# Kernel optimization log

Measured on AMD Instinct MI355X. Metric: run time of the kernel, lower is better.

## Reference

```python
import jax, jax.numpy as jnp
import numpy as np
from jax import lax

B, L, D_IN, D_H = 4096, 64, 256, 200


def setup_inputs() -> dict:
    key = jax.random.key(0)
    ks = jax.random.split(key, 9)
    s_in = 1.0 / np.sqrt(D_IN)
    s_cv = 1.0 / np.sqrt(D_IN * 4)
    return {
        "x": jax.random.normal(ks[0], (B, L, D_IN), dtype=jnp.float32),
        "Wq": jax.random.uniform(ks[1], (D_H, D_IN), jnp.float32, -s_in, s_in),
        "bq": jax.random.uniform(ks[2], (D_H,), jnp.float32, -s_in, s_in),
        "Wk": jax.random.uniform(ks[3], (D_H, D_IN), jnp.float32, -s_in, s_in),
        "bk": jax.random.uniform(ks[4], (D_H,), jnp.float32, -s_in, s_in),
        "Wv": jax.random.uniform(ks[5], (D_H, D_IN), jnp.float32, -s_in, s_in),
        "bv": jax.random.uniform(ks[6], (D_H,), jnp.float32, -s_in, s_in),
        "conv_w": jax.random.uniform(ks[7], (D_H, D_IN, 4), jnp.float32, -s_cv, s_cv),
        "conv_b": jax.random.uniform(ks[8], (D_H,), jnp.float32, -s_cv, s_cv),
    }


def reference(x, Wq, bq, Wk, bk, Wv, bv, conv_w, conv_b):
    # x: [B, L=64, 256]
    q = jax.nn.relu(jnp.einsum("bld,hd->blh", x, Wq) + bq)  # [B,L,200]
    k = jax.nn.relu(jnp.einsum("bld,hd->blh", x, Wk) + bk)  # relu commutes with permute
    v = jax.nn.relu(jnp.einsum("bld,hd->blh", x, Wv) + bv)
    scores = jnp.einsum("blh,bmh->blm", q, k)               # bmm(q, k^T): [B,L,L]
    soft = jax.nn.softmax(scores, axis=1)                   # NOTE: dim=1 (over queries), as in original
    self_att = jnp.einsum("blm,bmh->blh", soft, v)          # [B,L,200]
    b = x.shape[0]
    self_att = self_att.reshape(b, -1, 4, 16).mean(axis=2).reshape(b, 16, -1)  # [B,16,200]
    word_att = x.reshape(b, 256, 64)                        # [B, C=256, len=64]
    conv = lax.conv_general_dilated(
        word_att, conv_w, window_strides=(4,), padding="VALID",
        dimension_numbers=("NCH", "OIH", "NCH"))            # [B,200,16]
    conv = conv + conv_b[None, :, None]
    conv = conv.reshape(b, 16, -1)                          # raw reshape, as in original
    return conv + self_att                                  # [B,16,200]
```

## Files before the change

kernel.cpp:

```cpp
#include <hip/hip_runtime.h>

typedef _Float16 f16x8 __attribute__((ext_vector_type(8)));
typedef _Float16 f16x4 __attribute__((ext_vector_type(4)));
typedef float f32x4 __attribute__((ext_vector_type(4)));

#define THREADS 512

static __device__ __forceinline__ f32x4 MFMA(f16x8 a, f16x8 b, f32x4 c) {
  return __builtin_amdgcn_mfma_f32_16x16x32_f16(a, b, c, 0, 0, 0);
}

__global__ void wcvt(const float* __restrict__ Wq, const float* __restrict__ Wk,
                     const float* __restrict__ Wv, const float* __restrict__ cw,
                     const float* __restrict__ bq, const float* __restrict__ bk,
                     const float* __restrict__ bv,
                     _Float16* __restrict__ Wb,
                     _Float16* __restrict__ Wcb,
                     float* __restrict__ biasp) {
  int gt = blockIdx.x * blockDim.x + threadIdx.x;
  int gs = gridDim.x * blockDim.x;
  const int WN = 224 * 256;
  for (int i = gt; i < WN; i += gs) {
    int n = i >> 8;
    Wb[i]          = (n < 200) ? (_Float16)Wq[i] : (_Float16)0.f;
    Wb[WN + i]     = (n < 200) ? (_Float16)Wk[i] : (_Float16)0.f;
    Wb[2 * WN + i] = (n < 200) ? (_Float16)Wv[i] : (_Float16)0.f;
  }
  for (int i = gt; i < 224 * 1024; i += gs) {
    int o = i >> 10;
    Wcb[i] = (o < 200) ? (_Float16)cw[i] : (_Float16)0.f;
  }
  for (int i = gt; i < 224; i += gs) {
    biasp[i]       = (i < 200) ? bq[i] : 0.f;
    biasp[224 + i] = (i < 200) ? bk[i] : 0.f;
    biasp[448 + i] = (i < 200) ? bv[i] : 0.f;
  }
}

#define LDS_BYTES 151296

__global__ __launch_bounds__(THREADS, 2) void fused_kernel(
    const float* __restrict__ x, const _Float16* __restrict__ Wb,
    const _Float16* __restrict__ Wcb, const float* __restrict__ biasp,
    const float* __restrict__ convb, float* __restrict__ out) {
  extern __shared__ char smem[];
  _Float16* Xl = (_Float16*)smem;
  _Float16* Qs = (_Float16*)(smem + 33792);
  _Float16* Ks = (_Float16*)(smem + 63488);
  _Float16* Vt = (_Float16*)(smem + 93184);
  float* Sf    = (float*)(smem + 125440);
  _Float16* Sb = (_Float16*)(smem + 142080);
  float* SA    = (float*)(smem + 33792);
  float* Cv    = (float*)(smem + 125440);

  const int b = blockIdx.x;
  const int tid = threadIdx.x;
  const int lane = tid & 63;
  const int wave = tid >> 6;
  const int li = lane & 15;
  const int g = lane >> 4;

  const float* xb = x + (size_t)b * 16384;
  for (int i = tid; i < 4096; i += THREADS) {
    float4 v = ((const float4*)xb)[i];
    int e = i * 4;
    int l = e >> 8, d = e & 255;
    f16x4 h;
    h.x = (_Float16)v.x; h.y = (_Float16)v.y;
    h.z = (_Float16)v.z; h.w = (_Float16)v.w;
    *(f16x4*)(Xl + l * 264 + d) = h;
  }
  __syncthreads();

  for (int u = wave; u < 42; u += 8) {
    int p = u / 14, nt = u % 14;
    int n = nt * 16 + li;
    const _Float16* wrow = Wb + p * (224 * 256) + n * 256 + 8 * g;
    f16x8 bfr[8];
#pragma unroll
    for (int kk = 0; kk < 8; kk++) bfr[kk] = *(const f16x8*)(wrow + kk * 32);
    float bias = biasp[p * 224 + n];
    for (int m = 0; m < 4; m++) {
      f32x4 acc = {0.f, 0.f, 0.f, 0.f};
      const _Float16* arow = Xl + (m * 16 + li) * 264 + 8 * g;
#pragma unroll
      for (int kk = 0; kk < 8; kk++) {
        acc = MFMA(*(const f16x8*)(arow + kk * 32), bfr[kk], acc);
      }
#pragma unroll
      for (int r = 0; r < 4; r++) {
        int row = m * 16 + 4 * g + r;
        float v = acc[r] + bias;
        v = v > 0.f ? v : 0.f;
        _Float16 hv = (_Float16)v;
        if (p == 0) Qs[row * 232 + n] = hv;
        else if (p == 1) Ks[row * 232 + n] = hv;
        else Vt[n * 72 + row] = hv;
      }
    }
  }
  __syncthreads();

  for (int t = wave * 2; t < wave * 2 + 2; t++) {
    int mt = t >> 2, nt = t & 3;
    f32x4 acc = {0.f, 0.f, 0.f, 0.f};
    const _Float16* qrow = Qs + (mt * 16 + li) * 232 + 8 * g;
    const _Float16* krow = Ks + (nt * 16 + li) * 232 + 8 * g;
#pragma unroll
    for (int kk = 0; kk < 7; kk++) {
      acc = MFMA(*(const f16x8*)(qrow + kk * 32),
                 *(const f16x8*)(krow + kk * 32), acc);
    }
#pragma unroll
    for (int r = 0; r < 4; r++) {
      int row = mt * 16 + 4 * g + r;
      int col = nt * 16 + li;
      Sf[row * 65 + col] = acc[r];
    }
  }
  __syncthreads();

  {
    int m = tid >> 3, r = tid & 7;
    float vals[8];
    float mx = -1e30f;
#pragma unroll
    for (int i = 0; i < 8; i++) {
      float v = Sf[(r + 8 * i) * 65 + m];
      vals[i] = v;
      mx = fmaxf(mx, v);
    }
    mx = fmaxf(mx, __shfl_xor(mx, 1));
    mx = fmaxf(mx, __shfl_xor(mx, 2));
    mx = fmaxf(mx, __shfl_xor(mx, 4));
    float s = 0.f;
#pragma unroll
    for (int i = 0; i < 8; i++) {
      vals[i] = __expf(vals[i] - mx);
      s += vals[i];
    }
    s += __shfl_xor(s, 1);
    s += __shfl_xor(s, 2);
    s += __shfl_xor(s, 4);
    float inv = 1.0f / s;
#pragma unroll
    for (int i = 0; i < 8; i++)
      Sb[(r + 8 * i) * 72 + m] = (_Float16)(vals[i] * inv);
  }
  __syncthreads();

  for (int nt = wave; nt < 14; nt += 8) {
    int o = nt * 16 + li;
    const _Float16* wrow = Wcb + o * 1024 + 8 * g;
    f32x4 acc = {0.f, 0.f, 0.f, 0.f};
#pragma unroll 4
    for (int kk = 0; kk < 32; kk++) {
      int i1 = kk * 8 + 2 * g;
      int i2 = i1 + 1;
      union { f16x4 h[2]; f16x8 v; } af;
      af.h[0] = *(const f16x4*)(Xl + (i1 >> 2) * 264 + ((i1 & 3) << 6) + 4 * li);
      af.h[1] = *(const f16x4*)(Xl + (i2 >> 2) * 264 + ((i2 & 3) << 6) + 4 * li);
      acc = MFMA(af.v, *(const f16x8*)(wrow + kk * 32), acc);
    }
#pragma unroll
    for (int r = 0; r < 4; r++) Cv[(4 * g + r) * 226 + o] = acc[r];
  }

  for (int t = wave; t < 56; t += 8) {
    int mt = t / 14, nt = t % 14;
    f32x4 acc = {0.f, 0.f, 0.f, 0.f};
    const _Float16* arow = Sb + (mt * 16 + li) * 72 + 8 * g;
    const _Float16* brow = Vt + (nt * 16 + li) * 72 + 8 * g;
#pragma unroll
    for (int kk = 0; kk < 2; kk++) {
      acc = MFMA(*(const f16x8*)(arow + kk * 32),
                 *(const f16x8*)(brow + kk * 32), acc);
    }
#pragma unroll
    for (int r = 0; r < 4; r++)
      SA[(mt * 16 + 4 * g + r) * 228 + (nt * 16 + li)] = acc[r];
  }
  __syncthreads();

  float* ob = out + (size_t)b * 3200;
  for (int t = tid; t < 3200; t += THREADS) {
    int c = t >> 4, s = t & 15;
    float cv = Cv[s * 226 + c] + convb[c];
    float pool = 0.f;
#pragma unroll
    for (int j = 0; j < 4; j++) {
      int flat = c * 64 + j * 16 + s;
      int l = flat / 200;
      int h = flat - l * 200;
      pool += SA[l * 228 + h];
    }
    ob[t] = cv + 0.25f * pool;
  }
}

extern "C" void kernel_launch(void* const* d_in, const int* in_sizes, int n_in,
                              void* d_out, int out_size, void* d_ws, size_t ws_size,
                              hipStream_t stream) {
  const float* x  = (const float*)d_in[0];
  const float* Wq = (const float*)d_in[1];
  const float* bq = (const float*)d_in[2];
  const float* Wk = (const float*)d_in[3];
  const float* bk = (const float*)d_in[4];
  const float* Wv = (const float*)d_in[5];
  const float* bv = (const float*)d_in[6];
  const float* cw = (const float*)d_in[7];
  const float* cb = (const float*)d_in[8];

  char* ws = (char*)d_ws;
  _Float16* Wb  = (_Float16*)ws;
  _Float16* Wcb = (_Float16*)(ws + 344064);
  float* biasp  = (float*)(ws + 802816);

  hipLaunchKernelGGL(wcvt, dim3(512), dim3(256), 0, stream,
                     Wq, Wk, Wv, cw, bq, bk, bv, Wb, Wcb, biasp);

  hipFuncSetAttribute((const void*)fused_kernel,
                      hipFuncAttributeMaxDynamicSharedMemorySize, LDS_BYTES);
  hipLaunchKernelGGL(fused_kernel, dim3(4096), dim3(THREADS), LDS_BYTES, stream,
                     x, Wb, Wcb, biasp, cb, (float*)d_out);
}
```

Measured before the change: 532.8 us.

## Shrink LDS footprint via streamed QK slices and split V pass for higher occupancy

Restructures the fused kernel so Q/K projections are computed in 32-column slices whose scores accumulate in registers, instead of materialising full Q and K in LDS. V is computed in two halves, and the mean-pool is done with LDS atomics into a single output buffer. The X tile gets an XOR swizzle in place of padding. LDS use drops from about 148KB to about 77KB, and launch bounds go to 4 blocks per CU, to raise occupancy. In exchange it adds extra __syncthreads per slice, redundant X reads, and LDS atomic contention.

```diff
diff --git a/kernel.cpp b/kernel.cpp
--- a/kernel.cpp
+++ b/kernel.cpp
@@ -37,86 +37,93 @@
   }
 }
 
-#define LDS_BYTES 151296
-
-__global__ __launch_bounds__(THREADS, 2) void fused_kernel(
+#define LDS_BYTES 78592
+
+__global__ __launch_bounds__(THREADS, 4) void fused_kernel(
     const float* __restrict__ x, const _Float16* __restrict__ Wb,
     const _Float16* __restrict__ Wcb, const float* __restrict__ biasp,
     const float* __restrict__ convb, float* __restrict__ out) {
   extern __shared__ char smem[];
   _Float16* Xl = (_Float16*)smem;
-  _Float16* Qs = (_Float16*)(smem + 33792);
-  _Float16* Ks = (_Float16*)(smem + 63488);
-  _Float16* Vt = (_Float16*)(smem + 93184);
-  float* Sf    = (float*)(smem + 125440);
-  _Float16* Sb = (_Float16*)(smem + 142080);
-  float* SA    = (float*)(smem + 33792);
-  float* Cv    = (float*)(smem + 125440);
+  _Float16* QK = (_Float16*)(smem + 32768);
+  float*    Sf = (float*)(smem + 32768);
+  float*    Po = (float*)(smem + 32768);
+  _Float16* Sb = (_Float16*)(smem + 53248);
+  _Float16* Vt = (_Float16*)(smem + 62464);
 
   const int b = blockIdx.x;
   const int tid = threadIdx.x;
   const int lane = tid & 63;
   const int wave = tid >> 6;
   const int li = lane & 15;
-  const int g = lane >> 4;
+  const int g  = lane >> 4;
 
   const float* xb = x + (size_t)b * 16384;
-  for (int i = tid; i < 4096; i += THREADS) {
-    float4 v = ((const float4*)xb)[i];
-    int e = i * 4;
-    int l = e >> 8, d = e & 255;
+#pragma unroll
+  for (int jj = 0; jj < 8; jj++) {
+    int f = tid + 512 * jj;
+    float4 v = ((const float4*)xb)[f];
+    int l = f >> 6;
+    int c = (f & 63) >> 1;
+    int sub = (f & 1) * 4;
     f16x4 h;
     h.x = (_Float16)v.x; h.y = (_Float16)v.y;
     h.z = (_Float16)v.z; h.w = (_Float16)v.w;
-    *(f16x4*)(Xl + l * 264 + d) = h;
+    *(f16x4*)(Xl + l * 256 + ((c ^ (l & 7)) << 3) + sub) = h;
   }
   __syncthreads();
 
-  for (int u = wave; u < 42; u += 8) {
-    int p = u / 14, nt = u % 14;
-    int n = nt * 16 + li;
-    const _Float16* wrow = Wb + p * (224 * 256) + n * 256 + 8 * g;
-    f16x8 bfr[8];
-#pragma unroll
-    for (int kk = 0; kk < 8; kk++) bfr[kk] = *(const f16x8*)(wrow + kk * 32);
-    float bias = biasp[p * 224 + n];
-    for (int m = 0; m < 4; m++) {
+  f32x4 sacc0 = {0.f, 0.f, 0.f, 0.f};
+  f32x4 sacc1 = {0.f, 0.f, 0.f, 0.f};
+  const int t0 = 2 * wave;
+  for (int sl = 0; sl < 7; sl++) {
+#pragma unroll
+    for (int uu = 0; uu < 2; uu++) {
+      int u = 2 * wave + uu;
+      int p  = u >> 3;
+      int mt = (u & 7) >> 1;
+      int hh = u & 1;
+      int n = sl * 32 + hh * 16 + li;
+      const _Float16* wrow = Wb + p * 57344 + n * 256 + 8 * g;
       f32x4 acc = {0.f, 0.f, 0.f, 0.f};
-      const _Float16* arow = Xl + (m * 16 + li) * 264 + 8 * g;
+      int arow = mt * 16 + li;
 #pragma unroll
       for (int kk = 0; kk < 8; kk++) {
-        acc = MFMA(*(const f16x8*)(arow + kk * 32), bfr[kk], acc);
-      }
+        f16x8 af = *(const f16x8*)(Xl + arow * 256 + (((g + 4 * kk) ^ (arow & 7)) << 3));
+        f16x8 bf = *(const f16x8*)(wrow + 32 * kk);
+        acc = MFMA(af, bf, acc);
+      }
+      float bias = biasp[p * 224 + n];
 #pragma unroll
       for (int r = 0; r < 4; r++) {
-        int row = m * 16 + 4 * g + r;
         float v = acc[r] + bias;
         v = v > 0.f ? v : 0.f;
-        _Float16 hv = (_Float16)v;
-        if (p == 0) Qs[row * 232 + n] = hv;
-        else if (p == 1) Ks[row * 232 + n] = hv;
-        else Vt[n * 72 + row] = hv;
-      }
-    }
-  }
-  __syncthreads();
-
-  for (int t = wave * 2; t < wave * 2 + 2; t++) {
+        QK[p * 2560 + (mt * 16 + 4 * g + r) * 40 + hh * 16 + li] = (_Float16)v;
+      }
+    }
+    __syncthreads();
+    {
+      int mt = t0 >> 2, nt = t0 & 3;
+      f16x8 qa = *(const f16x8*)(QK + (mt * 16 + li) * 40 + 8 * g);
+      f16x8 kb = *(const f16x8*)(QK + 2560 + (nt * 16 + li) * 40 + 8 * g);
+      sacc0 = MFMA(qa, kb, sacc0);
+      int t1 = t0 + 1;
+      int mt1 = t1 >> 2, nt1 = t1 & 3;
+      f16x8 qa1 = *(const f16x8*)(QK + (mt1 * 16 + li) * 40 + 8 * g);
+      f16x8 kb1 = *(const f16x8*)(QK + 2560 + (nt1 * 16 + li) * 40 + 8 * g);
+      sacc1 = MFMA(qa1, kb1, sacc1);
+    }
+    __syncthreads();
+  }
+
+#pragma unroll
+  for (int tt = 0; tt < 2; tt++) {
+    int t = t0 + tt;
     int mt = t >> 2, nt = t & 3;
-    f32x4 acc = {0.f, 0.f, 0.f, 0.f};
-    const _Float16* qrow = Qs + (mt * 16 + li) * 232 + 8 * g;
-    const _Float16* krow = Ks + (nt * 16 + li) * 232 + 8 * g;
-#pragma unroll
-    for (int kk = 0; kk < 7; kk++) {
-      acc = MFMA(*(const f16x8*)(qrow + kk * 32),
-                 *(const f16x8*)(krow + kk * 32), acc);
-    }
-#pragma unroll
-    for (int r = 0; r < 4; r++) {
-      int row = mt * 16 + 4 * g + r;
-      int col = nt * 16 + li;
-      Sf[row * 65 + col] = acc[r];
-    }
+    f32x4 a = tt ? sacc1 : sacc0;
+#pragma unroll
+    for (int r = 0; r < 4; r++)
+      Sf[(mt * 16 + 4 * g + r) * 65 + nt * 16 + li] = a[r];
   }
   __syncthreads();
 
@@ -149,52 +156,83 @@
   }
   __syncthreads();
 
-  for (int nt = wave; nt < 14; nt += 8) {
-    int o = nt * 16 + li;
-    const _Float16* wrow = Wcb + o * 1024 + 8 * g;
-    f32x4 acc = {0.f, 0.f, 0.f, 0.f};
+  for (int half = 0; half < 2; half++) {
+    if (half == 0) {
+      for (int nt = wave; nt < 14; nt += 8) {
+        int o = nt * 16 + li;
+        const _Float16* wrow = Wcb + o * 1024 + 8 * g;
+        f32x4 acc = {0.f, 0.f, 0.f, 0.f};
 #pragma unroll 4
-    for (int kk = 0; kk < 32; kk++) {
-      int i1 = kk * 8 + 2 * g;
-      int i2 = i1 + 1;
-      union { f16x4 h[2]; f16x8 v; } af;
-      af.h[0] = *(const f16x4*)(Xl + (i1 >> 2) * 264 + ((i1 & 3) << 6) + 4 * li);
-      af.h[1] = *(const f16x4*)(Xl + (i2 >> 2) * 264 + ((i2 & 3) << 6) + 4 * li);
-      acc = MFMA(af.v, *(const f16x8*)(wrow + kk * 32), acc);
-    }
-#pragma unroll
-    for (int r = 0; r < 4; r++) Cv[(4 * g + r) * 226 + o] = acc[r];
-  }
-
-  for (int t = wave; t < 56; t += 8) {
-    int mt = t / 14, nt = t % 14;
-    f32x4 acc = {0.f, 0.f, 0.f, 0.f};
-    const _Float16* arow = Sb + (mt * 16 + li) * 72 + 8 * g;
-    const _Float16* brow = Vt + (nt * 16 + li) * 72 + 8 * g;
-#pragma unroll
-    for (int kk = 0; kk < 2; kk++) {
-      acc = MFMA(*(const f16x8*)(arow + kk * 32),
-                 *(const f16x8*)(brow + kk * 32), acc);
-    }
-#pragma unroll
-    for (int r = 0; r < 4; r++)
-      SA[(mt * 16 + 4 * g + r) * 228 + (nt * 16 + li)] = acc[r];
-  }
-  __syncthreads();
+        for (int kk = 0; kk < 32; kk++) {
+          int i1 = kk * 8 + 2 * g;
+          union { f16x4 h[2]; f16x8 v; } af;
+          {
+            int pos = 64 * i1 + 4 * li;
+            int row = pos >> 8, d = pos & 255;
+            af.h[0] = *(const f16x4*)(Xl + row * 256 +
+                        (((d >> 3) ^ (row & 7)) << 3) + (d & 7));
+          }
+          {
+            int pos = 64 * (i1 + 1) + 4 * li;
+            int row = pos >> 8, d = pos & 255;
+            af.h[1] = *(const f16x4*)(Xl + row * 256 +
+                        (((d >> 3) ^ (row & 7)) << 3) + (d & 7));
+          }
+          acc = MFMA(af.v, *(const f16x8*)(wrow + 32 * kk), acc);
+        }
+        if (o < 200) {
+#pragma unroll
+          for (int r = 0; r < 4; r++) Po[o * 17 + 4 * g + r] = acc[r];
+        }
+      }
+    }
+    for (int u = wave; u < 28; u += 8) {
+      int mt = u / 7, ht = u % 7;
+      int hloc = ht * 16 + li;
+      int n = half * 112 + hloc;
+      const _Float16* wrow = Wb + 2 * 57344 + n * 256 + 8 * g;
+      f32x4 acc = {0.f, 0.f, 0.f, 0.f};
+      int arow = mt * 16 + li;
+#pragma unroll
+      for (int kk = 0; kk < 8; kk++) {
+        f16x8 af = *(const f16x8*)(Xl + arow * 256 + (((g + 4 * kk) ^ (arow & 7)) << 3));
+        acc = MFMA(af, *(const f16x8*)(wrow + 32 * kk), acc);
+      }
+      float bias = biasp[448 + n];
+#pragma unroll
+      for (int r = 0; r < 4; r++) {
+        float v = acc[r] + bias;
+        v = v > 0.f ? v : 0.f;
+        Vt[hloc * 72 + mt * 16 + 4 * g + r] = (_Float16)v;
+      }
+    }
+    __syncthreads();
+    for (int u = wave; u < 28; u += 8) {
+      int mt = u / 7, ntl = u % 7;
+      f32x4 acc = {0.f, 0.f, 0.f, 0.f};
+#pragma unroll
+      for (int kk = 0; kk < 2; kk++) {
+        f16x8 pa = *(const f16x8*)(Sb + (mt * 16 + li) * 72 + 32 * kk + 8 * g);
+        f16x8 vb = *(const f16x8*)(Vt + (ntl * 16 + li) * 72 + 32 * kk + 8 * g);
+        acc = MFMA(pa, vb, acc);
+      }
+      int h = half * 112 + ntl * 16 + li;
+      if (h < 200) {
+#pragma unroll
+        for (int r = 0; r < 4; r++) {
+          int l = mt * 16 + 4 * g + r;
+          int flat = l * 200 + h;
+          atomicAdd(&Po[(flat >> 6) * 17 + (flat & 15)], 0.25f * acc[r]);
+        }
+      }
+    }
+    __syncthreads();
+  }
 
   float* ob = out + (size_t)b * 3200;
   for (int t = tid; t < 3200; t += THREADS) {
-    int c = t >> 4, s = t & 15;
-    float cv = Cv[s * 226 + c] + convb[c];
-    float pool = 0.f;
-#pragma unroll
-    for (int j = 0; j < 4; j++) {
-      int flat = c * 64 + j * 16 + s;
-      int l = flat / 200;
-      int h = flat - l * 200;
-      pool += SA[l * 228 + h];
-    }
-    ob[t] = cv + 0.25f * pool;
+    int c = t >> 4;
+    ob[t] = Po[c * 17 + (t & 15)] + convb[c];
   }
 }
 
```

New measurement: 1.079 ms. 102% more time.

## Split fused kernel into batched projection/conv kernel and separate attention kernel

Applied to the files above, without the earlier changes.

Replaces the single per-batch fused kernel with two kernels. The first processes four batch elements per block so each weight fragment loaded into registers is reused across four samples; it computes Q/K/V and the conv, and writes Q, K and V^T in fp16 to a large workspace and the conv result to the output. The second kernel reads Q/K/V back per batch element, runs the scores, softmax, PV and pooling with LDS atomics, and adds the result into the output. This cuts redundant weight reads and rebalances occupancy, at the cost of roughly 350 MB of extra global traffic for the Q/K/V round trip, a second launch, and a dependence on workspace size (otherwise the old fused path runs).

```diff
diff --git a/kernel.cpp b/kernel.cpp
--- a/kernel.cpp
+++ b/kernel.cpp
@@ -3,8 +3,6 @@
 typedef _Float16 f16x8 __attribute__((ext_vector_type(8)));
 typedef _Float16 f16x4 __attribute__((ext_vector_type(4)));
 typedef float f32x4 __attribute__((ext_vector_type(4)));
-
-#define THREADS 512
 
 static __device__ __forceinline__ f32x4 MFMA(f16x8 a, f16x8 b, f32x4 c) {
   return __builtin_amdgcn_mfma_f32_16x16x32_f16(a, b, c, 0, 0, 0);
@@ -37,9 +35,233 @@
   }
 }
 
-#define LDS_BYTES 151296
-
-__global__ __launch_bounds__(THREADS, 2) void fused_kernel(
+__global__ __launch_bounds__(512, 2) void k1_proj_conv(
+    const float* __restrict__ x, const _Float16* __restrict__ Wb,
+    const _Float16* __restrict__ Wcb, const float* __restrict__ biasp,
+    const float* __restrict__ convb,
+    _Float16* __restrict__ Qg, _Float16* __restrict__ Kg,
+    _Float16* __restrict__ Vtg, float* __restrict__ out) {
+  extern __shared__ char smem[];
+  _Float16* Xl = (_Float16*)smem;
+  const int tid = threadIdx.x, lane = tid & 63, wave = tid >> 6;
+  const int li = lane & 15, g = lane >> 4;
+  const int b0 = blockIdx.x * 4;
+
+  const float* xb = x + (size_t)b0 * 16384;
+#pragma unroll
+  for (int j = 0; j < 32; j++) {
+    int f = tid + 512 * j;
+    float4 v = ((const float4*)xb)[f];
+    int bt = f >> 12, rem = f & 4095, l = rem >> 6, c4 = rem & 63;
+    f16x4 h;
+    h.x = (_Float16)v.x; h.y = (_Float16)v.y;
+    h.z = (_Float16)v.z; h.w = (_Float16)v.w;
+    *(f16x4*)(Xl + bt * 16896 + l * 264 + c4 * 4) = h;
+  }
+  __syncthreads();
+
+  for (int i = 0; i < 7; i++) {
+    int u = wave + 8 * i;
+    if (u < 42) {
+      int p = u / 14, nt = u % 14, n = nt * 16 + li;
+      const _Float16* wrow = Wb + p * 57344 + n * 256 + 8 * g;
+      f16x8 bfr[8];
+#pragma unroll
+      for (int kk = 0; kk < 8; kk++) bfr[kk] = *(const f16x8*)(wrow + 32 * kk);
+      float bias = biasp[p * 224 + n];
+#pragma unroll
+      for (int bt = 0; bt < 4; bt++) {
+        const _Float16* xt = Xl + bt * 16896;
+        f32x4 acc[4] = {};
+#pragma unroll
+        for (int kk = 0; kk < 8; kk++) {
+#pragma unroll
+          for (int mt = 0; mt < 4; mt++) {
+            f16x8 af = *(const f16x8*)(xt + (mt * 16 + li) * 264 + 32 * kk + 8 * g);
+            acc[mt] = MFMA(af, bfr[kk], acc[mt]);
+          }
+        }
+        size_t bb = (size_t)(b0 + bt) * 14336;
+#pragma unroll
+        for (int mt = 0; mt < 4; mt++) {
+#pragma unroll
+          for (int r = 0; r < 4; r++) {
+            int l = mt * 16 + 4 * g + r;
+            float v = acc[mt][r] + bias;
+            _Float16 hv = (_Float16)(v > 0.f ? v : 0.f);
+            if (p == 0)      Qg[bb + l * 224 + n] = hv;
+            else if (p == 1) Kg[bb + l * 224 + n] = hv;
+            else             Vtg[bb + n * 64 + l] = hv;
+          }
+        }
+      }
+    } else {
+      int nt = u - 42, o = nt * 16 + li;
+      const _Float16* wrow = Wcb + o * 1024 + 8 * g;
+      f32x4 acc[4] = {};
+#pragma unroll 4
+      for (int kk = 0; kk < 32; kk++) {
+        f16x8 bf = *(const f16x8*)(wrow + 32 * kk);
+        int i1 = kk * 8 + 2 * g;
+        int i2 = i1 + 1;
+#pragma unroll
+        for (int bt = 0; bt < 4; bt++) {
+          const _Float16* xt = Xl + bt * 16896;
+          union { f16x4 h[2]; f16x8 v; } af;
+          af.h[0] = *(const f16x4*)(xt + (i1 >> 2) * 264 + ((i1 & 3) << 6) + 4 * li);
+          af.h[1] = *(const f16x4*)(xt + (i2 >> 2) * 264 + ((i2 & 3) << 6) + 4 * li);
+          acc[bt] = MFMA(af.v, bf, acc[bt]);
+        }
+      }
+      if (o < 200) {
+        float cb = convb[o];
+#pragma unroll
+        for (int bt = 0; bt < 4; bt++) {
+          float* ob = out + (size_t)(b0 + bt) * 3200 + o * 16;
+#pragma unroll
+          for (int r = 0; r < 4; r++) ob[4 * g + r] = acc[bt][r] + cb;
+        }
+      }
+    }
+  }
+}
+
+#define K3_LDS 68608
+__global__ __launch_bounds__(256, 2) void k3_attn(
+    const _Float16* __restrict__ Qg, const _Float16* __restrict__ Kg,
+    const _Float16* __restrict__ Vtg, float* __restrict__ out) {
+  extern __shared__ char smem[];
+  _Float16* Qs = (_Float16*)smem;
+  _Float16* Ks = (_Float16*)(smem + 29696);
+  float*    Sf = (float*)smem;
+  _Float16* Vt = (_Float16*)(smem + 29696);
+  _Float16* Sb = (_Float16*)(smem + 59392);
+  float*    Po = (float*)smem;
+
+  const int b = blockIdx.x;
+  const int tid = threadIdx.x, lane = tid & 63, wave = tid >> 6;
+  const int li = lane & 15, g = lane >> 4;
+  const size_t bb = (size_t)b * 14336;
+
+#pragma unroll
+  for (int i = 0; i < 7; i++) {
+    int j = tid + 256 * i;
+    f16x8 q = *(const f16x8*)(Qg + bb + j * 8);
+    int row = j / 28, col = (j % 28) * 8;
+    *(f16x8*)(Qs + row * 232 + col) = q;
+  }
+#pragma unroll
+  for (int i = 0; i < 7; i++) {
+    int j = tid + 256 * i;
+    f16x8 k = *(const f16x8*)(Kg + bb + j * 8);
+    int row = j / 28, col = (j % 28) * 8;
+    *(f16x8*)(Ks + row * 232 + col) = k;
+  }
+  f16x8 vreg[7];
+#pragma unroll
+  for (int i = 0; i < 7; i++)
+    vreg[i] = *(const f16x8*)(Vtg + bb + (tid + 256 * i) * 8);
+  __syncthreads();
+
+  f32x4 sacc[4] = {};
+  {
+    const int mt = wave;
+#pragma unroll
+    for (int kk = 0; kk < 7; kk++) {
+      f16x8 qa = *(const f16x8*)(Qs + (mt * 16 + li) * 232 + kk * 32 + 8 * g);
+#pragma unroll
+      for (int nt = 0; nt < 4; nt++) {
+        f16x8 kb = *(const f16x8*)(Ks + (nt * 16 + li) * 232 + kk * 32 + 8 * g);
+        sacc[nt] = MFMA(qa, kb, sacc[nt]);
+      }
+    }
+  }
+  __syncthreads();
+
+  {
+    const int mt = wave;
+#pragma unroll
+    for (int nt = 0; nt < 4; nt++)
+#pragma unroll
+      for (int r = 0; r < 4; r++)
+        Sf[(mt * 16 + 4 * g + r) * 65 + nt * 16 + li] = sacc[nt][r];
+  }
+#pragma unroll
+  for (int i = 0; i < 7; i++) {
+    int j = tid + 256 * i;
+    int h = j >> 3, c = j & 7;
+    *(f16x8*)(Vt + h * 64 + ((c ^ (h & 7)) << 3)) = vreg[i];
+  }
+  __syncthreads();
+
+  {
+    int m = tid >> 2, r4 = tid & 3;
+    float vals[16], mx = -1e30f;
+#pragma unroll
+    for (int i2 = 0; i2 < 16; i2++) {
+      float v = Sf[(r4 + 4 * i2) * 65 + m];
+      vals[i2] = v; mx = fmaxf(mx, v);
+    }
+    mx = fmaxf(mx, __shfl_xor(mx, 1));
+    mx = fmaxf(mx, __shfl_xor(mx, 2));
+    float s = 0.f;
+#pragma unroll
+    for (int i2 = 0; i2 < 16; i2++) { vals[i2] = __expf(vals[i2] - mx); s += vals[i2]; }
+    s += __shfl_xor(s, 1);
+    s += __shfl_xor(s, 2);
+    float inv = 1.f / s;
+#pragma unroll
+    for (int i2 = 0; i2 < 16; i2++)
+      Sb[(r4 + 4 * i2) * 72 + m] = (_Float16)(vals[i2] * inv);
+  }
+  __syncthreads();
+
+  for (int i = tid; i < 3400; i += 256) ((float*)smem)[i] = 0.f;
+  __syncthreads();
+
+  f16x8 pa[2][4];
+#pragma unroll
+  for (int kk = 0; kk < 2; kk++)
+#pragma unroll
+    for (int mt = 0; mt < 4; mt++)
+      pa[kk][mt] = *(const f16x8*)(Sb + (mt * 16 + li) * 72 + kk * 32 + 8 * g);
+
+  for (int ntl = wave; ntl < 14; ntl += 4) {
+    int h = ntl * 16 + li;
+    f16x8 vb[2];
+#pragma unroll
+    for (int kk = 0; kk < 2; kk++) {
+      int cm = 4 * kk + g;
+      vb[kk] = *(const f16x8*)(Vt + h * 64 + ((cm ^ (h & 7)) << 3));
+    }
+    f32x4 pacc[4] = {};
+#pragma unroll
+    for (int kk = 0; kk < 2; kk++)
+#pragma unroll
+      for (int mt = 0; mt < 4; mt++)
+        pacc[mt] = MFMA(pa[kk][mt], vb[kk], pacc[mt]);
+    if (h < 200) {
+#pragma unroll
+      for (int mt = 0; mt < 4; mt++)
+#pragma unroll
+        for (int r = 0; r < 4; r++) {
+          int l = mt * 16 + 4 * g + r;
+          int f = l * 200 + h;
+          atomicAdd(&Po[(f >> 6) * 17 + (f & 15)], 0.25f * pacc[mt][r]);
+        }
+    }
+  }
+  __syncthreads();
+
+  float* ob = out + (size_t)b * 3200;
+  for (int t = tid; t < 3200; t += 256) {
+    int c = t >> 4;
+    ob[t] += Po[c * 17 + (t & 15)];
+  }
+}
+
+#define FB_LDS 151296
+__global__ __launch_bounds__(512, 2) void fused_fallback(
     const float* __restrict__ x, const _Float16* __restrict__ Wb,
     const _Float16* __restrict__ Wcb, const float* __restrict__ biasp,
     const float* __restrict__ convb, float* __restrict__ out) {
@@ -61,7 +283,7 @@
   const int g = lane >> 4;
 
   const float* xb = x + (size_t)b * 16384;
-  for (int i = tid; i < 4096; i += THREADS) {
+  for (int i = tid; i < 4096; i += 512) {
     float4 v = ((const float4*)xb)[i];
     int e = i * 4;
     int l = e >> 8, d = e & 255;
@@ -75,7 +297,7 @@
   for (int u = wave; u < 42; u += 8) {
     int p = u / 14, nt = u % 14;
     int n = nt * 16 + li;
-    const _Float16* wrow = Wb + p * (224 * 256) + n * 256 + 8 * g;
+    const _Float16* wrow = Wb + p * 57344 + n * 256 + 8 * g;
     f16x8 bfr[8];
 #pragma unroll
     for (int kk = 0; kk < 8; kk++) bfr[kk] = *(const f16x8*)(wrow + kk * 32);
@@ -84,9 +306,7 @@
       f32x4 acc = {0.f, 0.f, 0.f, 0.f};
       const _Float16* arow = Xl + (m * 16 + li) * 264 + 8 * g;
 #pragma unroll
-      for (int kk = 0; kk < 8; kk++) {
-        acc = MFMA(*(const f16x8*)(arow + kk * 32), bfr[kk], acc);
-      }
+      for (int kk = 0; kk < 8; kk++) acc = MFMA(*(const f16x8*)(arow + kk * 32), bfr[kk], acc);
 #pragma unroll
       for (int r = 0; r < 4; r++) {
         int row = m * 16 + 4 * g + r;
@@ -107,16 +327,11 @@
     const _Float16* qrow = Qs + (mt * 16 + li) * 232 + 8 * g;
     const _Float16* krow = Ks + (nt * 16 + li) * 232 + 8 * g;
 #pragma unroll
-    for (int kk = 0; kk < 7; kk++) {
-      acc = MFMA(*(const f16x8*)(qrow + kk * 32),
-                 *(const f16x8*)(krow + kk * 32), acc);
-    }
-#pragma unroll
-    for (int r = 0; r < 4; r++) {
-      int row = mt * 16 + 4 * g + r;
-      int col = nt * 16 + li;
-      Sf[row * 65 + col] = acc[r];
-    }
+    for (int kk = 0; kk < 7; kk++)
+      acc = MFMA(*(const f16x8*)(qrow + kk * 32), *(const f16x8*)(krow + kk * 32), acc);
+#pragma unroll
+    for (int r = 0; r < 4; r++)
+      Sf[(mt * 16 + 4 * g + r) * 65 + nt * 16 + li] = acc[r];
   }
   __syncthreads();
 
@@ -135,10 +350,7 @@
     mx = fmaxf(mx, __shfl_xor(mx, 4));
     float s = 0.f;
 #pragma unroll
-    for (int i = 0; i < 8; i++) {
-      vals[i] = __expf(vals[i] - mx);
-      s += vals[i];
-    }
+    for (int i = 0; i < 8; i++) { vals[i] = __expf(vals[i] - mx); s += vals[i]; }
     s += __shfl_xor(s, 1);
     s += __shfl_xor(s, 2);
     s += __shfl_xor(s, 4);
@@ -160,7 +372,7 @@
       union { f16x4 h[2]; f16x8 v; } af;
       af.h[0] = *(const f16x4*)(Xl + (i1 >> 2) * 264 + ((i1 & 3) << 6) + 4 * li);
       af.h[1] = *(const f16x4*)(Xl + (i2 >> 2) * 264 + ((i2 & 3) << 6) + 4 * li);
-      acc = MFMA(af.v, *(const f16x8*)(wrow + kk * 32), acc);
+      acc = MFMA(af.v, *(const f16x8*)(wrow + 32 * kk), acc);
     }
 #pragma unroll
     for (int r = 0; r < 4; r++) Cv[(4 * g + r) * 226 + o] = acc[r];
@@ -172,10 +384,8 @@
     const _Float16* arow = Sb + (mt * 16 + li) * 72 + 8 * g;
     const _Float16* brow = Vt + (nt * 16 + li) * 72 + 8 * g;
 #pragma unroll
-    for (int kk = 0; kk < 2; kk++) {
-      acc = MFMA(*(const f16x8*)(arow + kk * 32),
-                 *(const f16x8*)(brow + kk * 32), acc);
-    }
+    for (int kk = 0; kk < 2; kk++)
+      acc = MFMA(*(const f16x8*)(arow + kk * 32), *(const f16x8*)(brow + kk * 32), acc);
 #pragma unroll
     for (int r = 0; r < 4; r++)
       SA[(mt * 16 + 4 * g + r) * 228 + (nt * 16 + li)] = acc[r];
@@ -183,7 +393,7 @@
   __syncthreads();
 
   float* ob = out + (size_t)b * 3200;
-  for (int t = tid; t < 3200; t += THREADS) {
+  for (int t = tid; t < 3200; t += 512) {
     int c = t >> 4, s = t & 15;
     float cv = Cv[s * 226 + c] + convb[c];
     float pool = 0.f;
@@ -219,8 +429,28 @@
   hipLaunchKernelGGL(wcvt, dim3(512), dim3(256), 0, stream,
                      Wq, Wk, Wv, cw, bq, bk, bv, Wb, Wcb, biasp);
 
-  hipFuncSetAttribute((const void*)fused_kernel,
-                      hipFuncAttributeMaxDynamicSharedMemorySize, LDS_BYTES);
-  hipLaunchKernelGGL(fused_kernel, dim3(4096), dim3(THREADS), LDS_BYTES, stream,
-                     x, Wb, Wcb, biasp, cb, (float*)d_out);
-}
+  const size_t QKV_BASE = 805888ull;
+  const size_t QKV_ONE  = 117440512ull;
+  const size_t NEED = QKV_BASE + 3ull * QKV_ONE;
+
+  if (ws_size >= NEED) {
+    _Float16* Qg  = (_Float16*)(ws + QKV_BASE);
+    _Float16* Kg  = (_Float16*)(ws + QKV_BASE + QKV_ONE);
+    _Float16* Vtg = (_Float16*)(ws + QKV_BASE + 2 * QKV_ONE);
+
+    hipFuncSetAttribute((const void*)k1_proj_conv,
+                        hipFuncAttributeMaxDynamicSharedMemorySize, 135168);
+    hipLaunchKernelGGL(k1_proj_conv, dim3(1024), dim3(512), 135168, stream,
+                       x, Wb, Wcb, biasp, cb, Qg, Kg, Vtg, (float*)d_out);
+
+    hipFuncSetAttribute((const void*)k3_attn,
+                        hipFuncAttributeMaxDynamicSharedMemorySize, K3_LDS);
+    hipLaunchKernelGGL(k3_attn, dim3(4096), dim3(256), K3_LDS, stream,
+                       Qg, Kg, Vtg, (float*)d_out);
+  } else {
+    hipFuncSetAttribute((const void*)fused_fallback,
+                        hipFuncAttributeMaxDynamicSharedMemorySize, FB_LDS);
+    hipLaunchKernelGGL(fused_fallback, dim3(4096), dim3(512), FB_LDS, stream,
+                       x, Wb, Wcb, biasp, cb, (float*)d_out);
+  }
+}
```

Result: slower. 624.7 us (+17.3%).

## Widen fused kernel to 1024 threads and overlap conv with QKV projections

Applied to the files above, without the earlier changes.

Doubles the block to 16 waves and puts the QKV projection tiles and the conv tiles into a single work loop, with one tile per wave, so the conv no longer runs as a separate phase. Each QKV tile now reuses one weight fragment across four row tiles, and V is stored transposed into a swizzled layout. The PV product accumulates the pooled self-attention result straight into a conv-initialised output buffer with LDS atomics, which removes the separate SA buffer and the final gather pass. LDS rises to about 161KB, so only one block fits per CU, and the atomics serialise some writes.

```diff
diff --git a/kernel.cpp b/kernel.cpp
--- a/kernel.cpp
+++ b/kernel.cpp
@@ -3,8 +3,6 @@
 typedef _Float16 f16x8 __attribute__((ext_vector_type(8)));
 typedef _Float16 f16x4 __attribute__((ext_vector_type(4)));
 typedef float f32x4 __attribute__((ext_vector_type(4)));
-
-#define THREADS 512
 
 static __device__ __forceinline__ f32x4 MFMA(f16x8 a, f16x8 b, f32x4 c) {
   return __builtin_amdgcn_mfma_f32_16x16x32_f16(a, b, c, 0, 0, 0);
@@ -37,9 +35,9 @@
   }
 }
 
-#define LDS_BYTES 151296
-
-__global__ __launch_bounds__(THREADS, 2) void fused_kernel(
+#define FU_LDS 161312
+
+__global__ __launch_bounds__(1024, 4) void fused_all(
     const float* __restrict__ x, const _Float16* __restrict__ Wb,
     const _Float16* __restrict__ Wcb, const float* __restrict__ biasp,
     const float* __restrict__ convb, float* __restrict__ out) {
@@ -48,10 +46,9 @@
   _Float16* Qs = (_Float16*)(smem + 33792);
   _Float16* Ks = (_Float16*)(smem + 63488);
   _Float16* Vt = (_Float16*)(smem + 93184);
-  float* Sf    = (float*)(smem + 125440);
-  _Float16* Sb = (_Float16*)(smem + 142080);
-  float* SA    = (float*)(smem + 33792);
-  float* Cv    = (float*)(smem + 125440);
+  float*    Sf = (float*)(smem + 121856);
+  _Float16* Sb = (_Float16*)(smem + 138496);
+  float*    Po = (float*)(smem + 147712);
 
   const int b = blockIdx.x;
   const int tid = threadIdx.x;
@@ -61,141 +58,172 @@
   const int g = lane >> 4;
 
   const float* xb = x + (size_t)b * 16384;
-  for (int i = tid; i < 4096; i += THREADS) {
-    float4 v = ((const float4*)xb)[i];
-    int e = i * 4;
-    int l = e >> 8, d = e & 255;
+#pragma unroll
+  for (int j = 0; j < 4; j++) {
+    int f = tid + 1024 * j;
+    float4 v = ((const float4*)xb)[f];
+    int l = f >> 6, c4 = f & 63;
     f16x4 h;
     h.x = (_Float16)v.x; h.y = (_Float16)v.y;
     h.z = (_Float16)v.z; h.w = (_Float16)v.w;
-    *(f16x4*)(Xl + l * 264 + d) = h;
-  }
-  __syncthreads();
-
-  for (int u = wave; u < 42; u += 8) {
-    int p = u / 14, nt = u % 14;
-    int n = nt * 16 + li;
-    const _Float16* wrow = Wb + p * (224 * 256) + n * 256 + 8 * g;
-    f16x8 bfr[8];
-#pragma unroll
-    for (int kk = 0; kk < 8; kk++) bfr[kk] = *(const f16x8*)(wrow + kk * 32);
-    float bias = biasp[p * 224 + n];
-    for (int m = 0; m < 4; m++) {
-      f32x4 acc = {0.f, 0.f, 0.f, 0.f};
-      const _Float16* arow = Xl + (m * 16 + li) * 264 + 8 * g;
+    *(f16x4*)(Xl + l * 264 + c4 * 4) = h;
+  }
+  __syncthreads();
+
+#pragma unroll 1
+  for (int u = wave; u < 56; u += 16) {
+    if (u < 28) {
+      int p = u / 14, nt = u % 14;
+      const _Float16* wrow = Wb + p * 57344 + (nt * 16 + li) * 256 + 8 * g;
+      _Float16* dst = (p == 0) ? Qs : Ks;
+      f32x4 acc[4] = {};
 #pragma unroll
       for (int kk = 0; kk < 8; kk++) {
-        acc = MFMA(*(const f16x8*)(arow + kk * 32), bfr[kk], acc);
-      }
-#pragma unroll
-      for (int r = 0; r < 4; r++) {
-        int row = m * 16 + 4 * g + r;
-        float v = acc[r] + bias;
-        v = v > 0.f ? v : 0.f;
-        _Float16 hv = (_Float16)v;
-        if (p == 0) Qs[row * 232 + n] = hv;
-        else if (p == 1) Ks[row * 232 + n] = hv;
-        else Vt[n * 72 + row] = hv;
-      }
-    }
-  }
-  __syncthreads();
-
-  for (int t = wave * 2; t < wave * 2 + 2; t++) {
-    int mt = t >> 2, nt = t & 3;
-    f32x4 acc = {0.f, 0.f, 0.f, 0.f};
-    const _Float16* qrow = Qs + (mt * 16 + li) * 232 + 8 * g;
-    const _Float16* krow = Ks + (nt * 16 + li) * 232 + 8 * g;
+        f16x8 aw = *(const f16x8*)(wrow + 32 * kk);
+#pragma unroll
+        for (int mt = 0; mt < 4; mt++) {
+          f16x8 bx = *(const f16x8*)(Xl + (mt * 16 + li) * 264 + 32 * kk + 8 * g);
+          acc[mt] = MFMA(aw, bx, acc[mt]);
+        }
+      }
+      float4 b4 = *(const float4*)(biasp + p * 224 + nt * 16 + 4 * g);
+#pragma unroll
+      for (int mt = 0; mt < 4; mt++) {
+        f16x4 hv;
+        float v0 = acc[mt][0] + b4.x; hv[0] = (_Float16)(v0 > 0.f ? v0 : 0.f);
+        float v1 = acc[mt][1] + b4.y; hv[1] = (_Float16)(v1 > 0.f ? v1 : 0.f);
+        float v2 = acc[mt][2] + b4.z; hv[2] = (_Float16)(v2 > 0.f ? v2 : 0.f);
+        float v3 = acc[mt][3] + b4.w; hv[3] = (_Float16)(v3 > 0.f ? v3 : 0.f);
+        *(f16x4*)(dst + (mt * 16 + li) * 232 + nt * 16 + 4 * g) = hv;
+      }
+    } else if (u < 42) {
+      int nt = u - 28;
+      const _Float16* wrow = Wb + 2 * 57344 + (nt * 16 + li) * 256 + 8 * g;
+      f32x4 acc[4] = {};
+#pragma unroll
+      for (int kk = 0; kk < 8; kk++) {
+        f16x8 bw = *(const f16x8*)(wrow + 32 * kk);
+#pragma unroll
+        for (int mt = 0; mt < 4; mt++) {
+          f16x8 ax = *(const f16x8*)(Xl + (mt * 16 + li) * 264 + 32 * kk + 8 * g);
+          acc[mt] = MFMA(ax, bw, acc[mt]);
+        }
+      }
+      float bias = biasp[448 + nt * 16 + li];
+      int h = nt * 16 + li;
+#pragma unroll
+      for (int mt = 0; mt < 4; mt++) {
+        f16x4 hv;
+#pragma unroll
+        for (int r = 0; r < 4; r++) {
+          float v = acc[mt][r] + bias;
+          hv[r] = (_Float16)(v > 0.f ? v : 0.f);
+        }
+        int c = mt * 2 + (g >> 1);
+        int sub = (g & 1) * 4;
+        *(f16x4*)(Vt + h * 64 + ((c ^ (h & 7)) << 3) + sub) = hv;
+      }
+    } else {
+      int nt = u - 42, o = nt * 16 + li;
+      const _Float16* wrow = Wcb + o * 1024 + 8 * g;
+      f32x4 acc = {};
+#pragma unroll 4
+      for (int kk = 0; kk < 32; kk++) {
+        int i1 = kk * 8 + 2 * g;
+        int i2 = i1 + 1;
+        union { f16x4 h[2]; f16x8 v; } af;
+        af.h[0] = *(const f16x4*)(Xl + (i1 >> 2) * 264 + ((i1 & 3) << 6) + 4 * li);
+        af.h[1] = *(const f16x4*)(Xl + (i2 >> 2) * 264 + ((i2 & 3) << 6) + 4 * li);
+        acc = MFMA(af.v, *(const f16x8*)(wrow + 32 * kk), acc);
+      }
+      if (o < 200) {
+        float cb = convb[o];
+#pragma unroll
+        for (int r = 0; r < 4; r++) Po[o * 17 + 4 * g + r] = acc[r] + cb;
+      }
+    }
+  }
+  __syncthreads();
+
+  {
+    int mt = wave >> 2, nt = wave & 3;
+    f32x4 sacc = {};
 #pragma unroll
     for (int kk = 0; kk < 7; kk++) {
-      acc = MFMA(*(const f16x8*)(qrow + kk * 32),
-                 *(const f16x8*)(krow + kk * 32), acc);
-    }
-#pragma unroll
-    for (int r = 0; r < 4; r++) {
-      int row = mt * 16 + 4 * g + r;
-      int col = nt * 16 + li;
-      Sf[row * 65 + col] = acc[r];
-    }
+      f16x8 qa = *(const f16x8*)(Qs + (mt * 16 + li) * 232 + kk * 32 + 8 * g);
+      f16x8 kb = *(const f16x8*)(Ks + (nt * 16 + li) * 232 + kk * 32 + 8 * g);
+      sacc = MFMA(qa, kb, sacc);
+    }
+#pragma unroll
+    for (int r = 0; r < 4; r++)
+      Sf[(mt * 16 + 4 * g + r) * 65 + nt * 16 + li] = sacc[r];
   }
   __syncthreads();
 
   {
-    int m = tid >> 3, r = tid & 7;
-    float vals[8];
-    float mx = -1e30f;
-#pragma unroll
-    for (int i = 0; i < 8; i++) {
-      float v = Sf[(r + 8 * i) * 65 + m];
-      vals[i] = v;
-      mx = fmaxf(mx, v);
+    int m = tid >> 4, r16 = tid & 15;
+    float vals[4], mx = -1e30f;
+#pragma unroll
+    for (int i = 0; i < 4; i++) {
+      float v = Sf[(r16 + 16 * i) * 65 + m];
+      vals[i] = v; mx = fmaxf(mx, v);
     }
     mx = fmaxf(mx, __shfl_xor(mx, 1));
     mx = fmaxf(mx, __shfl_xor(mx, 2));
     mx = fmaxf(mx, __shfl_xor(mx, 4));
+    mx = fmaxf(mx, __shfl_xor(mx, 8));
     float s = 0.f;
 #pragma unroll
-    for (int i = 0; i < 8; i++) {
-      vals[i] = __expf(vals[i] - mx);
-      s += vals[i];
-    }
+    for (int i = 0; i < 4; i++) { vals[i] = __expf(vals[i] - mx); s += vals[i]; }
     s += __shfl_xor(s, 1);
     s += __shfl_xor(s, 2);
     s += __shfl_xor(s, 4);
-    float inv = 1.0f / s;
-#pragma unroll
-    for (int i = 0; i < 8; i++)
-      Sb[(r + 8 * i) * 72 + m] = (_Float16)(vals[i] * inv);
-  }
-  __syncthreads();
-
-  for (int nt = wave; nt < 14; nt += 8) {
-    int o = nt * 16 + li;
-    const _Float16* wrow = Wcb + o * 1024 + 8 * g;
-    f32x4 acc = {0.f, 0.f, 0.f, 0.f};
-#pragma unroll 4
-    for (int kk = 0; kk < 32; kk++) {
-      int i1 = kk * 8 + 2 * g;
-      int i2 = i1 + 1;
-      union { f16x4 h[2]; f16x8 v; } af;
-      af.h[0] = *(const f16x4*)(Xl + (i1 >> 2) * 264 + ((i1 & 3) << 6) + 4 * li);
-      af.h[1] = *(const f16x4*)(Xl + (i2 >> 2) * 264 + ((i2 & 3) << 6) + 4 * li);
-      acc = MFMA(af.v, *(const f16x8*)(wrow + kk * 32), acc);
-    }
-#pragma unroll
-    for (int r = 0; r < 4; r++) Cv[(4 * g + r) * 226 + o] = acc[r];
-  }
-
-  for (int t = wave; t < 56; t += 8) {
-    int mt = t / 14, nt = t % 14;
-    f32x4 acc = {0.f, 0.f, 0.f, 0.f};
-    const _Float16* arow = Sb + (mt * 16 + li) * 72 + 8 * g;
-    const _Float16* brow = Vt + (nt * 16 + li) * 72 + 8 * g;
+    s += __shfl_xor(s, 8);
+    float inv = 1.f / s;
+#pragma unroll
+    for (int i = 0; i < 4; i++)
+      Sb[(r16 + 16 * i) * 72 + m] = (_Float16)(vals[i] * inv);
+  }
+  __syncthreads();
+
+  if (wave < 14) {
+    int ntl = wave;
+    int h = ntl * 16 + li;
+    f16x8 pa[2][4];
+#pragma unroll
+    for (int kk = 0; kk < 2; kk++)
+#pragma unroll
+      for (int m2 = 0; m2 < 4; m2++)
+        pa[kk][m2] = *(const f16x8*)(Sb + (m2 * 16 + li) * 72 + kk * 32 + 8 * g);
+    f16x8 vb[2];
 #pragma unroll
     for (int kk = 0; kk < 2; kk++) {
-      acc = MFMA(*(const f16x8*)(arow + kk * 32),
-                 *(const f16x8*)(brow + kk * 32), acc);
-    }
-#pragma unroll
-    for (int r = 0; r < 4; r++)
-      SA[(mt * 16 + 4 * g + r) * 228 + (nt * 16 + li)] = acc[r];
+      int cm = kk * 4 + g;
+      vb[kk] = *(const f16x8*)(Vt + h * 64 + ((cm ^ (h & 7)) << 3));
+    }
+    f32x4 pacc[4] = {};
+#pragma unroll
+    for (int kk = 0; kk < 2; kk++)
+#pragma unroll
+      for (int m2 = 0; m2 < 4; m2++)
+        pacc[m2] = MFMA(pa[kk][m2], vb[kk], pacc[m2]);
+    if (h < 200) {
+#pragma unroll
+      for (int m2 = 0; m2 < 4; m2++)
+#pragma unroll
+        for (int r = 0; r < 4; r++) {
+          int l = m2 * 16 + 4 * g + r;
+          int f = l * 200 + h;
+          atomicAdd(&Po[(f >> 6) * 17 + (f & 15)], 0.25f * pacc[m2][r]);
+        }
+    }
   }
   __syncthreads();
 
   float* ob = out + (size_t)b * 3200;
-  for (int t = tid; t < 3200; t += THREADS) {
-    int c = t >> 4, s = t & 15;
-    float cv = Cv[s * 226 + c] + convb[c];
-    float pool = 0.f;
-#pragma unroll
-    for (int j = 0; j < 4; j++) {
-      int flat = c * 64 + j * 16 + s;
-      int l = flat / 200;
-      int h = flat - l * 200;
-      pool += SA[l * 228 + h];
-    }
-    ob[t] = cv + 0.25f * pool;
-  }
+#pragma unroll 1
+  for (int t = tid; t < 3200; t += 1024)
+    ob[t] = Po[(t >> 4) * 17 + (t & 15)];
 }
 
 extern "C" void kernel_launch(void* const* d_in, const int* in_sizes, int n_in,
@@ -219,8 +247,8 @@
   hipLaunchKernelGGL(wcvt, dim3(512), dim3(256), 0, stream,
                      Wq, Wk, Wv, cw, bq, bk, bv, Wb, Wcb, biasp);
 
-  hipFuncSetAttribute((const void*)fused_kernel,
-                      hipFuncAttributeMaxDynamicSharedMemorySize, LDS_BYTES);
-  hipLaunchKernelGGL(fused_kernel, dim3(4096), dim3(THREADS), LDS_BYTES, stream,
+  hipFuncSetAttribute((const void*)fused_all,
+                      hipFuncAttributeMaxDynamicSharedMemorySize, FU_LDS);
+  hipLaunchKernelGGL(fused_all, dim3(4096), dim3(1024), FU_LDS, stream,
                      x, Wb, Wcb, biasp, cb, (float*)d_out);
 }
```

Result: slower. 702.3 us (+31.8%).
